# Performance work log

Hardware: AMD Instinct MI355X
Metric: run time of the kernel (lower is better)

The kernel has to match this reference:

```python
import jax, jax.numpy as jnp
import numpy as np
from jax import lax

A = 20          # alphabet size (input_size)
L = 512         # max_seq_length
CH = 8          # conv channels
N_LAYERS = 9    # log2(512) conv+pool stages


def setup_inputs() -> dict:
    key = jax.random.key(0)
    ks = jax.random.split(key, 6)
    B = 1024
    idx = jax.random.randint(ks[0], (B, L), 0, A)
    lens = jax.random.randint(ks[1], (B,), L // 4, L + 1)
    masks = jnp.arange(L)[None, :] < lens[:, None]            # [B, L] bool
    # one-hot sequences, zeroed at padded positions (so nonzero() skips them)
    x = jax.nn.one_hot(idx, A, dtype=jnp.float32) * masks[..., None].astype(jnp.float32)
    blosum = jax.random.normal(ks[2], (A, A), jnp.float32)
    blosum = (blosum + blosum.T) * 0.5                        # symmetric like BLOSUM
    lpm = blosum                                              # trainable copy
    pm = jnp.clip(blosum, 0.0)                                # clamp(min=0) constant
    std = jnp.ones((1,), jnp.float32)                         # Gaussian std for row decay
    w0 = jax.random.normal(ks[3], (CH, 1, 3), jnp.float32) * 0.3
    ws = jax.random.normal(ks[4], (N_LAYERS - 1, CH, CH, 3), jnp.float32) * 0.2
    return {"x": x, "masks": masks, "lpm": lpm, "pm": pm, "std": std, "w0": w0, "ws": ws}


def _shift_pos(m, k):
    # target index clamp(s + k, max=L-1): shift right by k, boundary index L-1
    # collects any source in the last k+1 positions (set semantics -> OR).
    head = jnp.zeros(m.shape[:-1] + (k,), dtype=bool)
    body = m[..., : L - k - 1]                                # targets k .. L-2
    last = jnp.any(m[..., L - 1 - k:], axis=-1, keepdims=True)
    return jnp.concatenate([head, body, last], axis=-1)


def _shift_neg(m, k):
    # target index clamp(s - k, min=0)
    first = jnp.any(m[..., : k + 1], axis=-1, keepdims=True)
    body = m[..., k + 1:]                                     # targets 1 .. L-1-k
    tail = jnp.zeros(m.shape[:-1] + (k,), dtype=bool)
    return jnp.concatenate([first, body, tail], axis=-1)


def _column(nz, lpm, pm):
    # Banded substitution scatter: each one-hot row i writes V[i, r] into row r
    # at the same (batch, seq) position. Original nested index_put loops collapse
    # to a single 20x20 matrix V applied via einsum (one-hot => no collisions).
    ii = jnp.arange(A)[:, None]
    rr = jnp.arange(A)[None, :]
    M = jnp.clip(lpm, 0.001, 1.0) * pm
    # up-writes: j in 1..18-i => i < r <= 18 ; down-writes: j in 1..i => r < i
    V = jnp.where((rr > ii) & (rr <= A - 2), M, 0.0) + jnp.where(rr < ii, M.T, 0.0)
    return jnp.einsum('bis,ir->brs', nz, V)


def _row(m, std):
    # Gaussian positional decay: writes exp(-k^2/(2 std^2)) at seq offsets +-k,
    # k = 1,2,3 in order (later k overwrites earlier at clamp collisions).
    row = jnp.zeros(m.shape, jnp.float32)
    for k in (1, 2, 3):
        mk = _shift_pos(m, k) | _shift_neg(m, k)
        vk = jnp.exp(-(k * k) / (2.0 * std * std))[0]
        row = jnp.where(mk, vk, row)
    return row


def _conv1d(h, w):
    # Conv1d(kernel=3, stride=1, pad=1, no bias)
    return lax.conv_general_dilated(h, w, (1,), [(1, 1)],
                                    dimension_numbers=('NCH', 'OIH', 'NCH'))


def _avgpool2(h):
    N, C, Lh = h.shape
    return h.reshape(N, C, Lh // 2, 2).mean(-1)


def reference(x, masks, lpm, pm, std, w0, ws):
    B = x.shape[0]
    xp = jnp.transpose(x, (0, 2, 1))          # [B, 20, L]
    m = xp != 0
    nz = m.astype(xp.dtype)
    h = xp + _column(nz, lpm, pm) + _row(m, std)
    h = h.reshape(B * A, 1, L)
    h = _avgpool2(_conv1d(h, w0))
    for i in range(N_LAYERS - 1):
        h = _avgpool2(_conv1d(h, ws[i]))
    return h.squeeze(-1).reshape(B, A, -1)    # [B, 20, 8]
```

## Files before the change

kernel.cpp:

```cpp
#include <hip/hip_runtime.h>
#include <math.h>

#define LSEQ 512
#define NA 20
#define NCH 8

__global__ __launch_bounds__(256) void wf_vt_kernel(
    const float* __restrict__ w0,
    const float* __restrict__ wsg,
    const float* __restrict__ lpm,
    const float* __restrict__ pm,
    float* __restrict__ wf,
    float* __restrict__ vtn)
{
    const int t = threadIdx.x;

    if (blockIdx.x == NCH) {
        for (int o = t; o < NA * NA; o += 256) {
            int j = o / NA, a = o % NA;
            float v = 0.f;
            if (a > j && a <= NA - 2)
                v += fminf(fmaxf(lpm[j * NA + a], 0.001f), 1.0f) * pm[j * NA + a];
            if (a < j)
                v += fminf(fmaxf(lpm[a * NA + j], 0.001f), 1.0f) * pm[a * NA + j];
            vtn[o] = v;
        }
        return;
    }

    const int r = blockIdx.x;

    __shared__ float gA[NCH * 256];
    __shared__ float gB[NCH * 256];
    __shared__ float4 s_e[NCH * NCH];

    if (t < NCH) gA[t * 256] = (t == r) ? 1.f : 0.f;
    __syncthreads();

    int P = 1;
    for (int step = 0; step < 8; ++step) {
        const int li = 7 - step;
        if (t < 64) {
            const int co = t >> 3, ci = t & 7;
            const float* wp = wsg + li * 192 + co * 24 + ci * 3;
            const float a0 = wp[0], a1 = wp[1], a2 = wp[2];
            s_e[co * 8 + ci] = make_float4(a0 + a1, a2, a1 + a2, a0);
        }
        __syncthreads();
        const float* gi = (step & 1) ? gB : gA;
        float* go = (step & 1) ? gA : gB;
        for (int it = t; it < NCH * P; it += 256) {
            const int ci = it >> step;
            const int p = it & (P - 1);
            float accE = 0.f, accO = 0.f;
#pragma unroll
            for (int co = 0; co < NCH; ++co) {
                const float g0 = gi[co * 256 + p];
                const float gm = (p > 0) ? gi[co * 256 + p - 1] : 0.f;
                const float gp = (p + 1 < P) ? gi[co * 256 + p + 1] : 0.f;
                const float4 e = s_e[co * 8 + ci];
                accE += e.x * g0 + e.y * gm;
                accO += e.z * g0 + e.w * gp;
            }
            *(float2*)(go + ci * 256 + 2 * p) = make_float2(0.5f * accE, 0.5f * accO);
        }
        __syncthreads();
        P <<= 1;
    }

    {
        const int p = t;
        float accE = 0.f, accO = 0.f;
#pragma unroll
        for (int co = 0; co < NCH; ++co) {
            const float g0 = gA[co * 256 + p];
            const float gm = (p > 0) ? gA[co * 256 + p - 1] : 0.f;
            const float gp = (p < 255) ? gA[co * 256 + p + 1] : 0.f;
            const float q0 = w0[co * 3 + 0], q1 = w0[co * 3 + 1], q2 = w0[co * 3 + 2];
            accE += (q0 + q1) * g0 + q2 * gm;
            accO += (q1 + q2) * g0 + q0 * gp;
        }
        *(float2*)(wf + r * 512 + 2 * p) = make_float2(0.5f * accE, 0.5f * accO);
    }
}

__global__ __launch_bounds__(256) void main_kernel(
    const float* __restrict__ x,
    const float* __restrict__ vtn,
    const float* __restrict__ g_std,
    const float* __restrict__ wf,
    float* __restrict__ out)
{
    const int b = blockIdx.x;
    const int t = threadIdx.x;
    const int c = t & 7;
    const int seg = t >> 3;
    const int w = t >> 6;
    const int lane = t & 63;

    __shared__ __align__(16) float s_h[NA * 512];
    __shared__ __align__(16) float s_vtn[NA * NA];
    __shared__ float s_part[4 * NA * NCH];
    __shared__ unsigned char s_idx[LSEQ];

    float4 wr[4];
#pragma unroll
    for (int k = 0; k < 4; ++k)
        wr[k] = *(const float4*)(wf + c * 512 + seg * 4 + 128 * k);

    if (t < NA * NA / 4) ((float4*)s_vtn)[t] = ((const float4*)vtn)[t];

    const float4* xb = (const float4*)(x + (size_t)b * LSEQ * NA);
#pragma unroll
    for (int rep = 0; rep < 2; ++rep) {
        int s = t + rep * 256;
        int id = 255;
#pragma unroll
        for (int q = 0; q < 5; ++q) {
            float4 v = xb[s * 5 + q];
            if (v.x > .5f) id = 4 * q + 0;
            if (v.y > .5f) id = 4 * q + 1;
            if (v.z > .5f) id = 4 * q + 2;
            if (v.w > .5f) id = 4 * q + 3;
        }
        s_idx[s] = (unsigned char)id;
    }
    __syncthreads();

    const float stdv = g_std[0];
    const float inv2s2 = 1.f / (2.f * stdv * stdv);
    const float vks[3] = {__expf(-1.f * inv2s2), __expf(-4.f * inv2s2), __expf(-9.f * inv2s2)};

    for (int s = t; s < LSEQ; s += 256) {
        const int ai = s_idx[s];
        const bool valid = ai < NA;
#pragma unroll
        for (int a = 0; a < NA; ++a) {
            float v = valid ? (s_vtn[ai * NA + a] + (a == ai ? 1.f : 0.f)) : 0.f;
            s_h[a * 512 + s] = v;
        }
#pragma unroll
        for (int k = 1; k <= 3; ++k) {
            const float add = vks[k - 1];
            if (s == LSEQ - 1) {
                for (int u = LSEQ - 1 - k; u <= LSEQ - 1; ++u) {
                    int tg = s_idx[u];
                    if (tg < NA)
                        s_h[tg * 512 + s] =
                            (valid ? s_vtn[ai * NA + tg] + (tg == ai ? 1.f : 0.f) : 0.f) + add;
                }
            } else if (s >= k) {
                int tg = s_idx[s - k];
                if (tg < NA)
                    s_h[tg * 512 + s] =
                        (valid ? s_vtn[ai * NA + tg] + (tg == ai ? 1.f : 0.f) : 0.f) + add;
            }
            if (s == 0) {
                for (int u = 0; u <= k; ++u) {
                    int tg = s_idx[u];
                    if (tg < NA)
                        s_h[tg * 512 + s] =
                            (valid ? s_vtn[ai * NA + tg] + (tg == ai ? 1.f : 0.f) : 0.f) + add;
                }
            } else if (s + k < LSEQ) {
                int tg = s_idx[s + k];
                if (tg < NA)
                    s_h[tg * 512 + s] =
                        (valid ? s_vtn[ai * NA + tg] + (tg == ai ? 1.f : 0.f) : 0.f) + add;
            }
        }
    }
    __syncthreads();

#pragma unroll 1
    for (int a = 0; a < NA; ++a) {
        const float* hb = s_h + a * 512 + seg * 4;
        float acc = 0.f;
#pragma unroll
        for (int k = 0; k < 4; ++k) {
            float4 hv = *(const float4*)(hb + 128 * k);
            acc += hv.x * wr[k].x + hv.y * wr[k].y + hv.z * wr[k].z + hv.w * wr[k].w;
        }
        acc += __shfl_xor(acc, 8);
        acc += __shfl_xor(acc, 16);
        acc += __shfl_xor(acc, 32);
        if ((lane >> 3) == 0) s_part[w * (NA * NCH) + a * NCH + c] = acc;
    }
    __syncthreads();

    if (t < NA * NCH)
        out[(size_t)b * (NA * NCH) + t] =
            s_part[t] + s_part[160 + t] + s_part[320 + t] + s_part[480 + t];
}

extern "C" void kernel_launch(void* const* d_in, const int* in_sizes, int n_in,
                              void* d_out, int out_size, void* d_ws, size_t ws_size,
                              hipStream_t stream) {
    const float* x    = (const float*)d_in[0];
    const float* lpm  = (const float*)d_in[2];
    const float* pm   = (const float*)d_in[3];
    const float* stdp = (const float*)d_in[4];
    const float* w0   = (const float*)d_in[5];
    const float* wsg  = (const float*)d_in[6];
    float* out = (float*)d_out;

    const int B = in_sizes[0] / (LSEQ * NA);

    float* vtn = (float*)d_ws;
    float* wfb = (float*)d_ws + 1024;

    wf_vt_kernel<<<dim3(NCH + 1), dim3(256), 0, stream>>>(w0, wsg, lpm, pm, wfb, vtn);
    main_kernel<<<dim3(B), dim3(256), 0, stream>>>(x, vtn, stdp, wfb, out);
}
```

Baseline: 112.7 us.

## Process sequence in two halves to halve shared memory and raise occupancy

```diff
diff --git a/kernel.cpp b/kernel.cpp
--- a/kernel.cpp
+++ b/kernel.cpp
@@ -84,7 +84,7 @@
     }
 }
 
-__global__ __launch_bounds__(256) void main_kernel(
+__global__ __launch_bounds__(256, 4) void main_kernel(
     const float* __restrict__ x,
     const float* __restrict__ vtn,
     const float* __restrict__ g_std,
@@ -98,7 +98,7 @@
     const int w = t >> 6;
     const int lane = t & 63;
 
-    __shared__ __align__(16) float s_h[NA * 512];
+    __shared__ __align__(16) float s_h[NA * 256];
     __shared__ __align__(16) float s_vtn[NA * NA];
     __shared__ float s_part[4 * NA * NCH];
     __shared__ unsigned char s_idx[LSEQ];
@@ -131,60 +131,73 @@
     const float inv2s2 = 1.f / (2.f * stdv * stdv);
     const float vks[3] = {__expf(-1.f * inv2s2), __expf(-4.f * inv2s2), __expf(-9.f * inv2s2)};
 
-    for (int s = t; s < LSEQ; s += 256) {
-        const int ai = s_idx[s];
-        const bool valid = ai < NA;
-#pragma unroll
-        for (int a = 0; a < NA; ++a) {
-            float v = valid ? (s_vtn[ai * NA + a] + (a == ai ? 1.f : 0.f)) : 0.f;
-            s_h[a * 512 + s] = v;
-        }
-#pragma unroll
-        for (int k = 1; k <= 3; ++k) {
-            const float add = vks[k - 1];
-            if (s == LSEQ - 1) {
-                for (int u = LSEQ - 1 - k; u <= LSEQ - 1; ++u) {
-                    int tg = s_idx[u];
+    float acc[NA];
+#pragma unroll
+    for (int a = 0; a < NA; ++a) acc[a] = 0.f;
+
+    for (int half = 0; half < 2; ++half) {
+        {
+            const int s = 256 * half + t;
+            const int ai = s_idx[s];
+            const bool valid = ai < NA;
+#pragma unroll
+            for (int a = 0; a < NA; ++a) {
+                float v = valid ? (s_vtn[ai * NA + a] + (a == ai ? 1.f : 0.f)) : 0.f;
+                s_h[a * 256 + t] = v;
+            }
+#pragma unroll
+            for (int k = 1; k <= 3; ++k) {
+                const float add = vks[k - 1];
+                if (s == LSEQ - 1) {
+                    for (int u = LSEQ - 1 - k; u <= LSEQ - 1; ++u) {
+                        int tg = s_idx[u];
+                        if (tg < NA)
+                            s_h[tg * 256 + t] =
+                                (valid ? s_vtn[ai * NA + tg] + (tg == ai ? 1.f : 0.f) : 0.f) + add;
+                    }
+                } else if (s >= k) {
+                    int tg = s_idx[s - k];
                     if (tg < NA)
-                        s_h[tg * 512 + s] =
+                        s_h[tg * 256 + t] =
                             (valid ? s_vtn[ai * NA + tg] + (tg == ai ? 1.f : 0.f) : 0.f) + add;
                 }
-            } else if (s >= k) {
-                int tg = s_idx[s - k];
-                if (tg < NA)
-                    s_h[tg * 512 + s] =
-                        (valid ? s_vtn[ai * NA + tg] + (tg == ai ? 1.f : 0.f) : 0.f) + add;
-            }
-            if (s == 0) {
-                for (int u = 0; u <= k; ++u) {
-                    int tg = s_idx[u];
+                if (s == 0) {
+                    for (int u = 0; u <= k; ++u) {
+                        int tg = s_idx[u];
+                        if (tg < NA)
+                            s_h[tg * 256 + t] =
+                                (valid ? s_vtn[ai * NA + tg] + (tg == ai ? 1.f : 0.f) : 0.f) + add;
+                    }
+                } else if (s + k < LSEQ) {
+                    int tg = s_idx[s + k];
                     if (tg < NA)
-                        s_h[tg * 512 + s] =
+                        s_h[tg * 256 + t] =
                             (valid ? s_vtn[ai * NA + tg] + (tg == ai ? 1.f : 0.f) : 0.f) + add;
                 }
-            } else if (s + k < LSEQ) {
-                int tg = s_idx[s + k];
-                if (tg < NA)
-                    s_h[tg * 512 + s] =
-                        (valid ? s_vtn[ai * NA + tg] + (tg == ai ? 1.f : 0.f) : 0.f) + add;
-            }
-        }
-    }
-    __syncthreads();
-
-#pragma unroll 1
+            }
+        }
+        __syncthreads();
+
+#pragma unroll
+        for (int a = 0; a < NA; ++a) {
+            const float* hb = s_h + a * 256 + seg * 4;
+#pragma unroll
+            for (int kl = 0; kl < 2; ++kl) {
+                const int k = 2 * half + kl;
+                float4 hv = *(const float4*)(hb + 128 * kl);
+                acc[a] += hv.x * wr[k].x + hv.y * wr[k].y + hv.z * wr[k].z + hv.w * wr[k].w;
+            }
+        }
+        __syncthreads();
+    }
+
+#pragma unroll
     for (int a = 0; a < NA; ++a) {
-        const float* hb = s_h + a * 512 + seg * 4;
-        float acc = 0.f;
-#pragma unroll
-        for (int k = 0; k < 4; ++k) {
-            float4 hv = *(const float4*)(hb + 128 * k);
-            acc += hv.x * wr[k].x + hv.y * wr[k].y + hv.z * wr[k].z + hv.w * wr[k].w;
-        }
-        acc += __shfl_xor(acc, 8);
-        acc += __shfl_xor(acc, 16);
-        acc += __shfl_xor(acc, 32);
-        if ((lane >> 3) == 0) s_part[w * (NA * NCH) + a * NCH + c] = acc;
+        float v = acc[a];
+        v += __shfl_xor(v, 8);
+        v += __shfl_xor(v, 16);
+        v += __shfl_xor(v, 32);
+        if ((lane >> 3) == 0) s_part[w * (NA * NCH) + a * NCH + c] = v;
     }
     __syncthreads();
 
```

New measurement: 194.8 us. 1.73x slower.
